# Kernel tuning notes

Measured on AMD Instinct MI355X. Metric: run time of the kernel, lower is better.

The kernel has to match this reference:

```python
import jax, jax.numpy as jnp
import numpy as np

CE_W, TRI_W, CEN_W, ALN_W, BAL_W = 1.0, 1.0, 0.0005, 0.5, 0.1
LS_EPS = 0.1      # label smoothing
MARGIN = 0.3      # triplet margin
F_ALPHA, F_GAMMA = 0.25, 2.0


def setup_inputs() -> dict:
    key = jax.random.key(0)
    ks = jax.random.split(key, 7)
    B, C, D = 1024, 8000, 2048
    return {
        "logits": jax.random.normal(ks[0], (B, C), jnp.float32),
        "features": jax.random.normal(ks[1], (B, D), jnp.float32),
        "feat_rgb": jax.random.normal(ks[2], (B, D), jnp.float32),
        "feat_ir": jax.random.normal(ks[3], (B, D), jnp.float32),
        "modality_weights": jax.random.uniform(ks[4], (B, 2), jnp.float32),
        "centers": jax.random.uniform(ks[5], (C, D), jnp.float32, -1.0, 1.0),
        "labels": jax.random.randint(ks[6], (B,), 0, 64),
    }


def reference(logits, features, feat_rgb, feat_ir, modality_weights, centers, labels):
    B, C = logits.shape
    logp = jax.nn.log_softmax(logits, axis=-1)                      # [B, C]
    logp_y = jnp.take_along_axis(logp, labels[:, None], axis=1)[:, 0]
    # CrossEntropy with label smoothing 0.1 (torch semantics)
    ce = jnp.mean(-(1.0 - LS_EPS) * logp_y - LS_EPS * jnp.mean(logp, axis=-1))
    # Focal loss (faithful to source: uses logpt, so term is <= 0)
    ce_ns = -logp_y
    pt = jnp.exp(-ce_ns)
    focal = jnp.mean(F_ALPHA * (1.0 - pt) ** F_GAMMA * (-ce_ns))
    # Batch-hard triplet (vectorized replacement for per-row python loop)
    sq = jnp.sum(features ** 2, axis=1)
    d2 = jnp.maximum(sq[:, None] + sq[None, :] - 2.0 * (features @ features.T), 0.0)
    dist = jnp.where(d2 > 0, jnp.sqrt(jnp.where(d2 > 0, d2, 1.0)), 0.0)  # safe sqrt
    eq = labels[:, None] == labels[None, :]
    eye = jnp.eye(B, dtype=bool)
    pos_mask = eq & ~eye
    neg_mask = ~eq
    hp = jnp.max(jnp.where(pos_mask, dist, -1.0), axis=1)   # hardest positive
    hn = jnp.min(jnp.where(neg_mask, dist, 1e9), axis=1)    # hardest negative
    valid = jnp.any(pos_mask, axis=1) & jnp.any(neg_mask, axis=1)
    tl = jax.nn.relu(hp - hn + MARGIN)
    triplet = jnp.sum(jnp.where(valid, tl, 0.0)) / jnp.maximum(jnp.sum(valid), 1)
    # Center loss (centers gathered and detached)
    cen = jnp.mean((features - jax.lax.stop_gradient(centers[labels])) ** 2)
    # Modality alignment (single rgb-ir pair): mean(1 - cos)
    f1 = feat_rgb / jnp.maximum(jnp.linalg.norm(feat_rgb, axis=1, keepdims=True), 1e-12)
    f2 = feat_ir / jnp.maximum(jnp.linalg.norm(feat_ir, axis=1, keepdims=True), 1e-12)
    align = jnp.mean(1.0 - jnp.sum(f1 * f2, axis=1))
    # Modality balance: max_entropy - entropy
    ent = jnp.mean(-jnp.sum(modality_weights * jnp.log(modality_weights + 1e-8), axis=1))
    balance = jnp.log(jnp.float32(modality_weights.shape[1])) - ent
    # Modality consistency: mse to detached mean over modalities
    mean_feat = jax.lax.stop_gradient(0.5 * (feat_rgb + feat_ir))
    cons = 0.5 * (jnp.mean((feat_rgb - mean_feat) ** 2) + jnp.mean((feat_ir - mean_feat) ** 2))
    total = (CE_W * (0.7 * ce + 0.3 * focal) + TRI_W * triplet + CEN_W * cen
             + ALN_W * align + BAL_W * balance + 0.1 * cons)
    return jnp.stack([total, ce, focal, triplet, cen, align, balance, cons])
```

## Files before the change

kernel.cpp:

```cpp
#include <hip/hip_runtime.h>
#include <math.h>

#define NB 1024
#define NC 8000
#define ND 2048

#define WS_SQ   0
#define WS_CE   1024
#define WS_FO   2048
#define WS_CEN  3072
#define WS_AL   4096
#define WS_CO   5120
#define WS_HPM  6144
#define WS_HNM  22528
#define WS_FB_BYTES 262144

#define NDIST 512

typedef __attribute__((ext_vector_type(8))) short bf16x8;
typedef __attribute__((ext_vector_type(4))) float f32x4;
#define GLOB __attribute__((address_space(1)))
#define LDSP __attribute__((address_space(3)))

__device__ inline unsigned short f2bf(float f) {
    unsigned u = __float_as_uint(f);
    u += 0x7FFFu + ((u >> 16) & 1u);
    return (unsigned short)(u >> 16);
}

__global__ __launch_bounds__(256) void k_feat(const float* __restrict__ F,
                                              const float* __restrict__ RGB,
                                              const float* __restrict__ IR,
                                              const float* __restrict__ CEN,
                                              const int* __restrict__ labels,
                                              float* __restrict__ ws,
                                              unsigned short* __restrict__ Fb) {
    const int tid = threadIdx.x;
    const int lane = tid & 63, wid = tid >> 6;
    const int row = blockIdx.x * 4 + wid;
    const float4* f4 = (const float4*)(F + (size_t)row * ND);
    const float4* c4 = (const float4*)(CEN + (size_t)labels[row] * ND);
    const float4* r4 = (const float4*)(RGB + (size_t)row * ND);
    const float4* g4 = (const float4*)(IR + (size_t)row * ND);
    ushort4* fb4 = (ushort4*)(Fb + (size_t)row * ND);

    float s_ff = 0, s_fc = 0, s_rr = 0, s_ii = 0, s_ri = 0, s_dd = 0;
#pragma unroll 4
    for (int t = 0; t < (ND / 4) / 64; ++t) {
        const int q = t * 64 + lane;
        float4 f = f4[q], c = c4[q], r = r4[q], g = g4[q];
        ushort4 h;
        h.x = f2bf(f.x); h.y = f2bf(f.y); h.z = f2bf(f.z); h.w = f2bf(f.w);
        fb4[q] = h;
        float fa[4] = {f.x, f.y, f.z, f.w};
        float ca[4] = {c.x, c.y, c.z, c.w};
        float ra[4] = {r.x, r.y, r.z, r.w};
        float ga[4] = {g.x, g.y, g.z, g.w};
#pragma unroll
        for (int k = 0; k < 4; ++k) {
            s_ff = fmaf(fa[k], fa[k], s_ff);
            float d = fa[k] - ca[k];
            s_fc = fmaf(d, d, s_fc);
            s_rr = fmaf(ra[k], ra[k], s_rr);
            s_ii = fmaf(ga[k], ga[k], s_ii);
            s_ri = fmaf(ra[k], ga[k], s_ri);
            float e = ra[k] - ga[k];
            s_dd = fmaf(e, e, s_dd);
        }
    }
#pragma unroll
    for (int off = 32; off > 0; off >>= 1) {
        s_ff += __shfl_down(s_ff, off);
        s_fc += __shfl_down(s_fc, off);
        s_rr += __shfl_down(s_rr, off);
        s_ii += __shfl_down(s_ii, off);
        s_ri += __shfl_down(s_ri, off);
        s_dd += __shfl_down(s_dd, off);
    }
    if (lane == 0) {
        ws[WS_SQ + row] = s_ff;
        ws[WS_CEN + row] = s_fc;
        float nr = fmaxf(sqrtf(s_rr), 1e-12f);
        float ni = fmaxf(sqrtf(s_ii), 1e-12f);
        ws[WS_AL + row] = 1.0f - s_ri / (nr * ni);
        ws[WS_CO + row] = s_dd;
    }
}

__global__ __launch_bounds__(256) void k_main(const unsigned short* __restrict__ Fb,
                                              const float* __restrict__ logits,
                                              const int* __restrict__ labels,
                                              float* __restrict__ ws) {
    __shared__ __align__(16) unsigned short As[2][32 * 64];
    __shared__ __align__(16) unsigned short Bs[2][64 * 64];
    __shared__ int lr[32], lc[64];
    __shared__ float sqr[32], sqc[64], hpl[32], hnl[32];
    __shared__ float rs[4], rsx[4];

    const int tid = threadIdx.x;
    const int lane = tid & 63, wid = tid >> 6;

    if (blockIdx.x < NDIST) {
        const int cb = blockIdx.x & 15;
        const int row0 = (blockIdx.x >> 4) << 5;
        const int col0 = cb << 6;
        const float* sq = ws + WS_SQ;

        if (tid < 32) {
            lr[tid] = labels[row0 + tid];
            sqr[tid] = sq[row0 + tid];
            hpl[tid] = -1.0f;
            hnl[tid] = 1e9f;
        } else if (tid >= 64 && tid < 128) {
            int t = tid - 64;
            lc[t] = labels[col0 + t];
            sqc[t] = sq[col0 + t];
        }

        const int r8 = lane >> 3;
        const int sl = lane & 7;
        const int soEl = ((sl ^ r8) * 8);

#define STAGE(IT, BUF) do {                                                              \
    const int k0_ = (IT) * 64;                                                           \
    __builtin_amdgcn_global_load_lds(                                                    \
        (const GLOB unsigned int*)(Fb + (size_t)(row0 + wid * 8 + r8) * ND + k0_ + soEl),\
        (LDSP unsigned int*)&As[BUF][(wid * 8) * 64], 16, 0, 0);                         \
    _Pragma("unroll")                                                                    \
    for (int t = 0; t < 2; ++t) {                                                        \
        const int rb_ = wid * 16 + t * 8;                                                \
        __builtin_amdgcn_global_load_lds(                                                \
            (const GLOB unsigned int*)(Fb + (size_t)(col0 + rb_ + r8) * ND + k0_ + soEl),\
            (LDSP unsigned int*)&Bs[BUF][rb_ * 64], 16, 0, 0);                           \
    }                                                                                    \
} while (0)

        const int wr = wid >> 1, wc = wid & 1;
        f32x4 acc[2] = {};

        STAGE(0, 0);
        int cur = 0;
        for (int it = 0; it < ND / 64; ++it) {
            __syncthreads();
            if (it + 1 < ND / 64) STAGE(it + 1, cur ^ 1);
            const char* Ab = (const char*)&As[cur][0];
            const char* Bb = (const char*)&Bs[cur][0];
#pragma unroll
            for (int kk = 0; kk < 2; ++kk) {
                const int kb = kk * 64 + (lane >> 4) * 16;
                const int xo = (lane & 7) << 4;
                const int rt = wr * 16 + (lane & 15);
                bf16x8 a = *(const bf16x8*)(Ab + rt * 128 + (kb ^ xo));
                bf16x8 b[2];
#pragma unroll
                for (int ni = 0; ni < 2; ++ni) {
                    const int ct = wc * 32 + ni * 16 + (lane & 15);
                    b[ni] = *(const bf16x8*)(Bb + ct * 128 + (kb ^ xo));
                }
#pragma unroll
                for (int ni = 0; ni < 2; ++ni)
                    acc[ni] = __builtin_amdgcn_mfma_f32_16x16x32_bf16(a, b[ni], acc[ni], 0, 0, 0);
            }
            cur ^= 1;
        }
#undef STAGE

#pragma unroll
        for (int reg = 0; reg < 4; ++reg) {
            const int rt = wr * 16 + (lane >> 4) * 4 + reg;
            const int lbr = lr[rt];
            const float sr = sqr[rt];
            float myhp = -1.0f, myhn = 1e9f;
#pragma unroll
            for (int ni = 0; ni < 2; ++ni) {
                const int ct = wc * 32 + ni * 16 + (lane & 15);
                float d2 = sr + sqc[ct] - 2.0f * acc[ni][reg];
                float dist = sqrtf(fmaxf(d2, 0.0f));
                if (row0 + rt != col0 + ct) {
                    if (lbr == lc[ct]) myhp = fmaxf(myhp, dist);
                    else               myhn = fminf(myhn, dist);
                }
            }
#pragma unroll
            for (int off = 1; off < 16; off <<= 1) {
                myhp = fmaxf(myhp, __shfl_xor(myhp, off, 16));
                myhn = fminf(myhn, __shfl_xor(myhn, off, 16));
            }
            if ((lane & 15) == 0) {
                atomicMax((int*)&hpl[rt], __float_as_int(myhp));
                atomicMin((int*)&hnl[rt], __float_as_int(myhn));
            }
        }
        __syncthreads();
        if (tid < 32) {
            ws[WS_HPM + (size_t)(row0 + tid) * 16 + cb] = hpl[tid];
            ws[WS_HNM + (size_t)(row0 + tid) * 16 + cb] = hnl[tid];
        }
    } else {
        const int row = blockIdx.x - NDIST;
        const float* x = logits + (size_t)row * NC;
        const float4* x4 = (const float4*)x;
        float xl = 0.0f;
        if (tid == 0) xl = x[labels[row]];

        float s = 0.0f, sx = 0.0f;
        for (int q = tid; q < NC / 4; q += 256) {
            float4 v = x4[q];
            float vv[4] = {v.x, v.y, v.z, v.w};
#pragma unroll
            for (int c = 0; c < 4; ++c) {
                sx += vv[c];
                s += __expf(vv[c]);
            }
        }
#pragma unroll
        for (int off = 32; off > 0; off >>= 1) {
            s  += __shfl_down(s, off);
            sx += __shfl_down(sx, off);
        }
        if (lane == 0) { rs[wid] = s; rsx[wid] = sx; }
        __syncthreads();
        if (tid == 0) {
            s = rs[0] + rs[1] + rs[2] + rs[3];
            sx = rsx[0] + rsx[1] + rsx[2] + rsx[3];
            const float lse = __logf(s);
            const float logp_y = xl - lse;
            const float mean_logp = sx * (1.0f / NC) - lse;
            const float pt = __expf(logp_y);
            ws[WS_CE + row] = -(1.0f - 0.1f) * logp_y - 0.1f * mean_logp;
            ws[WS_FO + row] = 0.25f * (1.0f - pt) * (1.0f - pt) * logp_y;
        }
    }
}

__global__ __launch_bounds__(256) void k_fin(const float* __restrict__ mw,
                                             float* __restrict__ ws,
                                             float* __restrict__ out) {
    const int tid = threadIdx.x;
    float sum_tl = 0.0f, ent = 0.0f, sce = 0.0f, sfo = 0.0f;
    float scen = 0.0f, sal = 0.0f, sco = 0.0f;
    int cnt = 0;
#pragma unroll
    for (int t = 0; t < 4; ++t) {
        const int i = tid + t * 256;
        const float4* hp4 = (const float4*)(ws + WS_HPM + (size_t)i * 16);
        const float4* hn4 = (const float4*)(ws + WS_HNM + (size_t)i * 16);
        float h1 = -1.0f, h2 = 1e9f;
#pragma unroll
        for (int c = 0; c < 4; ++c) {
            float4 p = hp4[c], n = hn4[c];
            h1 = fmaxf(h1, fmaxf(fmaxf(p.x, p.y), fmaxf(p.z, p.w)));
            h2 = fminf(h2, fminf(fminf(n.x, n.y), fminf(n.z, n.w)));
        }
        if (h1 >= 0.0f && h2 < 1e8f) { sum_tl += fmaxf(h1 - h2 + 0.3f, 0.0f); cnt++; }
        sce += ws[WS_CE + i];
        sfo += ws[WS_FO + i];
        scen += ws[WS_CEN + i];
        sal += ws[WS_AL + i];
        sco += ws[WS_CO + i];
        float w0 = mw[2 * i], w1 = mw[2 * i + 1];
        ent -= w0 * __logf(w0 + 1e-8f) + w1 * __logf(w1 + 1e-8f);
    }
#pragma unroll
    for (int off = 32; off > 0; off >>= 1) {
        sum_tl += __shfl_down(sum_tl, off);
        ent += __shfl_down(ent, off);
        sce += __shfl_down(sce, off);
        sfo += __shfl_down(sfo, off);
        scen += __shfl_down(scen, off);
        sal += __shfl_down(sal, off);
        sco += __shfl_down(sco, off);
        cnt += __shfl_down(cnt, off);
    }
    __shared__ float red[4][7];
    __shared__ int rc[4];
    const int lane = tid & 63, wid = tid >> 6;
    if (lane == 0) {
        red[wid][0] = sum_tl; red[wid][1] = ent; red[wid][2] = sce; red[wid][3] = sfo;
        red[wid][4] = scen; red[wid][5] = sal; red[wid][6] = sco;
        rc[wid] = cnt;
    }
    __syncthreads();
    if (tid == 0) {
#pragma unroll
        for (int w = 1; w < 4; ++w) {
            red[0][0] += red[w][0]; red[0][1] += red[w][1]; red[0][2] += red[w][2];
            red[0][3] += red[w][3]; red[0][4] += red[w][4]; red[0][5] += red[w][5];
            red[0][6] += red[w][6];
            rc[0] += rc[w];
        }
        const float ce = red[0][2] * (1.0f / NB);
        const float focal = red[0][3] * (1.0f / NB);
        const float triplet = red[0][0] / (float)(rc[0] > 0 ? rc[0] : 1);
        const float cen = red[0][4] * (1.0f / ((float)NB * ND));
        const float align = red[0][5] * (1.0f / NB);
        const float balance = logf(2.0f) - red[0][1] * (1.0f / NB);
        const float cons = 0.25f * red[0][6] * (1.0f / ((float)NB * ND));
        const float total = 1.0f * (0.7f * ce + 0.3f * focal) + 1.0f * triplet
                          + 0.0005f * cen + 0.5f * align + 0.1f * balance + 0.1f * cons;
        out[0] = total; out[1] = ce; out[2] = focal; out[3] = triplet;
        out[4] = cen; out[5] = align; out[6] = balance; out[7] = cons;
    }
}

extern "C" void kernel_launch(void* const* d_in, const int* in_sizes, int n_in,
                              void* d_out, int out_size, void* d_ws, size_t ws_size,
                              hipStream_t stream) {
    const float* logits   = (const float*)d_in[0];
    const float* features = (const float*)d_in[1];
    const float* feat_rgb = (const float*)d_in[2];
    const float* feat_ir  = (const float*)d_in[3];
    const float* mw       = (const float*)d_in[4];
    const float* centers  = (const float*)d_in[5];
    const int*   labels   = (const int*)d_in[6];
    float* ws  = (float*)d_ws;
    unsigned short* Fb = (unsigned short*)((char*)d_ws + WS_FB_BYTES);
    float* out = (float*)d_out;

    k_feat<<<dim3(NB / 4), dim3(256), 0, stream>>>(features, feat_rgb, feat_ir,
                                                   centers, labels, ws, Fb);
    k_main<<<dim3(NDIST + NB), dim3(256), 0, stream>>>(Fb, logits, labels, ws);
    k_fin<<<dim3(1), dim3(256), 0, stream>>>(mw, ws, out);
}
```

Measured before the change: 42.49 us.

## Load MFMA operands directly from global memory and remap distance blocks per XCD

Drops the double-buffered LDS staging of the bf16 Gram-matrix tiles. Each lane now reads its bf16x8 fragments straight from global memory, relying on L2/cache reuse instead of shared memory. Distance block indices are also remapped so blocks landing on the same XCD share row and column panels, to improve L2 locality. This removes the per-iteration barriers and LDS traffic, but each loaded fragment feeds only two MFMAs, so the loop may become bound on global load latency.

```diff
diff --git a/kernel.cpp b/kernel.cpp
--- a/kernel.cpp
+++ b/kernel.cpp
@@ -19,8 +19,6 @@
 
 typedef __attribute__((ext_vector_type(8))) short bf16x8;
 typedef __attribute__((ext_vector_type(4))) float f32x4;
-#define GLOB __attribute__((address_space(1)))
-#define LDSP __attribute__((address_space(3)))
 
 __device__ inline unsigned short f2bf(float f) {
     unsigned u = __float_as_uint(f);
@@ -91,8 +89,6 @@
                                               const float* __restrict__ logits,
                                               const int* __restrict__ labels,
                                               float* __restrict__ ws) {
-    __shared__ __align__(16) unsigned short As[2][32 * 64];
-    __shared__ __align__(16) unsigned short Bs[2][64 * 64];
     __shared__ int lr[32], lc[64];
     __shared__ float sqr[32], sqc[64], hpl[32], hnl[32];
     __shared__ float rs[4], rsx[4];
@@ -101,9 +97,11 @@
     const int lane = tid & 63, wid = tid >> 6;
 
     if (blockIdx.x < NDIST) {
-        const int cb = blockIdx.x & 15;
-        const int row0 = (blockIdx.x >> 4) << 5;
-        const int col0 = cb << 6;
+        const int d = blockIdx.x;
+        const int xcd = d & 7, loc = d >> 3;
+        const int rp = (xcd >> 1) * 8 + (loc & 7);
+        const int cb = (xcd & 1) * 8 + (loc >> 3);
+        const int row0 = rp << 5, col0 = cb << 6;
         const float* sq = ws + WS_SQ;
 
         if (tid < 32) {
@@ -117,53 +115,23 @@
             sqc[t] = sq[col0 + t];
         }
 
-        const int r8 = lane >> 3;
-        const int sl = lane & 7;
-        const int soEl = ((sl ^ r8) * 8);
-
-#define STAGE(IT, BUF) do {                                                              \
-    const int k0_ = (IT) * 64;                                                           \
-    __builtin_amdgcn_global_load_lds(                                                    \
-        (const GLOB unsigned int*)(Fb + (size_t)(row0 + wid * 8 + r8) * ND + k0_ + soEl),\
-        (LDSP unsigned int*)&As[BUF][(wid * 8) * 64], 16, 0, 0);                         \
-    _Pragma("unroll")                                                                    \
-    for (int t = 0; t < 2; ++t) {                                                        \
-        const int rb_ = wid * 16 + t * 8;                                                \
-        __builtin_amdgcn_global_load_lds(                                                \
-            (const GLOB unsigned int*)(Fb + (size_t)(col0 + rb_ + r8) * ND + k0_ + soEl),\
-            (LDSP unsigned int*)&Bs[BUF][rb_ * 64], 16, 0, 0);                           \
-    }                                                                                    \
-} while (0)
-
         const int wr = wid >> 1, wc = wid & 1;
+        const int lane15 = lane & 15, kq = lane >> 4;
+        const unsigned short* pa  = Fb + (size_t)(row0 + wr * 16 + lane15) * ND + kq * 8;
+        const unsigned short* pb0 = Fb + (size_t)(col0 + wc * 32 + lane15) * ND + kq * 8;
+        const unsigned short* pb1 = pb0 + 16 * ND;
+
         f32x4 acc[2] = {};
-
-        STAGE(0, 0);
-        int cur = 0;
-        for (int it = 0; it < ND / 64; ++it) {
-            __syncthreads();
-            if (it + 1 < ND / 64) STAGE(it + 1, cur ^ 1);
-            const char* Ab = (const char*)&As[cur][0];
-            const char* Bb = (const char*)&Bs[cur][0];
-#pragma unroll
-            for (int kk = 0; kk < 2; ++kk) {
-                const int kb = kk * 64 + (lane >> 4) * 16;
-                const int xo = (lane & 7) << 4;
-                const int rt = wr * 16 + (lane & 15);
-                bf16x8 a = *(const bf16x8*)(Ab + rt * 128 + (kb ^ xo));
-                bf16x8 b[2];
-#pragma unroll
-                for (int ni = 0; ni < 2; ++ni) {
-                    const int ct = wc * 32 + ni * 16 + (lane & 15);
-                    b[ni] = *(const bf16x8*)(Bb + ct * 128 + (kb ^ xo));
-                }
-#pragma unroll
-                for (int ni = 0; ni < 2; ++ni)
-                    acc[ni] = __builtin_amdgcn_mfma_f32_16x16x32_bf16(a, b[ni], acc[ni], 0, 0, 0);
-            }
-            cur ^= 1;
-        }
-#undef STAGE
+#pragma unroll 8
+        for (int it = 0; it < ND / 32; ++it) {
+            bf16x8 a  = *(const bf16x8*)(pa  + it * 32);
+            bf16x8 b0 = *(const bf16x8*)(pb0 + it * 32);
+            bf16x8 b1 = *(const bf16x8*)(pb1 + it * 32);
+            acc[0] = __builtin_amdgcn_mfma_f32_16x16x32_bf16(a, b0, acc[0], 0, 0, 0);
+            acc[1] = __builtin_amdgcn_mfma_f32_16x16x32_bf16(a, b1, acc[1], 0, 0, 0);
+        }
+
+        __syncthreads();
 
 #pragma unroll
         for (int reg = 0; reg < 4; ++reg) {
@@ -317,8 +285,8 @@
     unsigned short* Fb = (unsigned short*)((char*)d_ws + WS_FB_BYTES);
     float* out = (float*)d_out;
 
-    k_feat<<<dim3(NB / 4), dim3(256), 0, stream>>>(features, feat_rgb, feat_ir,
-                                                   centers, labels, ws, Fb);
+    k_feat<<<dim3(256), dim3(256), 0, stream>>>(features, feat_rgb, feat_ir,
+                                                centers, labels, ws, Fb);
     k_main<<<dim3(NDIST + NB), dim3(256), 0, stream>>>(Fb, logits, labels, ws);
     k_fin<<<dim3(1), dim3(256), 0, stream>>>(mw, ws, out);
 }
```

Result: slower. 64.05 us (+50.8%).

## Exploit Gram-matrix symmetry with 64x64 upper-triangular tiles and padded bf16 rows

Applied to the files above, without the earlier changes.

The distance GEMM now computes only the upper-triangular 64x64 tiles (136 blocks instead of 512 32x64 blocks). Each off-diagonal tile also reduces along columns to produce the transposed row's hardest positive and negative. The bf16 feature rows are padded to a stride of 2080 to avoid channel or bank conflicts. The pipeline uses explicit vmcnt waits and raw barriers. This halves the GEMM work but leaves fewer, heavier blocks and adds a second per-tile reduction pass.

```diff
diff --git a/kernel.cpp b/kernel.cpp
--- a/kernel.cpp
+++ b/kernel.cpp
@@ -4,6 +4,7 @@
 #define NB 1024
 #define NC 8000
 #define ND 2048
+#define FBS 2080
 
 #define WS_SQ   0
 #define WS_CE   1024
@@ -15,7 +16,8 @@
 #define WS_HNM  22528
 #define WS_FB_BYTES 262144
 
-#define NDIST 512
+#define NTILES 136
+#define NT     32
 
 typedef __attribute__((ext_vector_type(8))) short bf16x8;
 typedef __attribute__((ext_vector_type(4))) float f32x4;
@@ -42,7 +44,7 @@
     const float4* c4 = (const float4*)(CEN + (size_t)labels[row] * ND);
     const float4* r4 = (const float4*)(RGB + (size_t)row * ND);
     const float4* g4 = (const float4*)(IR + (size_t)row * ND);
-    ushort4* fb4 = (ushort4*)(Fb + (size_t)row * ND);
+    ushort4* fb4 = (ushort4*)(Fb + (size_t)row * FBS);
 
     float s_ff = 0, s_fc = 0, s_rr = 0, s_ii = 0, s_ri = 0, s_dd = 0;
 #pragma unroll 4
@@ -91,30 +93,34 @@
                                               const float* __restrict__ logits,
                                               const int* __restrict__ labels,
                                               float* __restrict__ ws) {
-    __shared__ __align__(16) unsigned short As[2][32 * 64];
+    __shared__ __align__(16) unsigned short As[2][64 * 64];
     __shared__ __align__(16) unsigned short Bs[2][64 * 64];
-    __shared__ int lr[32], lc[64];
-    __shared__ float sqr[32], sqc[64], hpl[32], hnl[32];
+    __shared__ int lr[64], lc[64];
+    __shared__ float sqr[64], sqc[64];
+    __shared__ float hplR[64], hnlR[64], hplC[64], hnlC[64];
     __shared__ float rs[4], rsx[4];
 
     const int tid = threadIdx.x;
     const int lane = tid & 63, wid = tid >> 6;
 
-    if (blockIdx.x < NDIST) {
-        const int cb = blockIdx.x & 15;
-        const int row0 = (blockIdx.x >> 4) << 5;
-        const int col0 = cb << 6;
+    if (blockIdx.x < NTILES) {
+        int rem = blockIdx.x, rp = 0;
+        while (rem >= 16 - rp) { rem -= 16 - rp; rp++; }
+        const int cp = rp + rem;
+        const int row0 = rp << 6, col0 = cp << 6;
         const float* sq = ws + WS_SQ;
 
-        if (tid < 32) {
+        if (tid < 64) {
             lr[tid] = labels[row0 + tid];
             sqr[tid] = sq[row0 + tid];
-            hpl[tid] = -1.0f;
-            hnl[tid] = 1e9f;
-        } else if (tid >= 64 && tid < 128) {
+            hplR[tid] = -1.0f;
+            hnlR[tid] = 1e9f;
+        } else if (tid < 128) {
             int t = tid - 64;
             lc[t] = labels[col0 + t];
             sqc[t] = sq[col0 + t];
+            hplC[t] = -1.0f;
+            hnlC[t] = 1e9f;
         }
 
         const int r8 = lane >> 3;
@@ -123,81 +129,133 @@
 
 #define STAGE(IT, BUF) do {                                                              \
     const int k0_ = (IT) * 64;                                                           \
-    __builtin_amdgcn_global_load_lds(                                                    \
-        (const GLOB unsigned int*)(Fb + (size_t)(row0 + wid * 8 + r8) * ND + k0_ + soEl),\
-        (LDSP unsigned int*)&As[BUF][(wid * 8) * 64], 16, 0, 0);                         \
     _Pragma("unroll")                                                                    \
     for (int t = 0; t < 2; ++t) {                                                        \
         const int rb_ = wid * 16 + t * 8;                                                \
         __builtin_amdgcn_global_load_lds(                                                \
-            (const GLOB unsigned int*)(Fb + (size_t)(col0 + rb_ + r8) * ND + k0_ + soEl),\
+            (const GLOB unsigned int*)(Fb + (size_t)(row0 + rb_ + r8) * FBS + k0_ + soEl),\
+            (LDSP unsigned int*)&As[BUF][rb_ * 64], 16, 0, 0);                           \
+        __builtin_amdgcn_global_load_lds(                                                \
+            (const GLOB unsigned int*)(Fb + (size_t)(col0 + rb_ + r8) * FBS + k0_ + soEl),\
             (LDSP unsigned int*)&Bs[BUF][rb_ * 64], 16, 0, 0);                           \
     }                                                                                    \
 } while (0)
 
         const int wr = wid >> 1, wc = wid & 1;
-        f32x4 acc[2] = {};
+        f32x4 acc[2][2] = {};
 
         STAGE(0, 0);
         int cur = 0;
-        for (int it = 0; it < ND / 64; ++it) {
-            __syncthreads();
-            if (it + 1 < ND / 64) STAGE(it + 1, cur ^ 1);
+#pragma unroll 1
+        for (int it = 0; it < NT; ++it) {
+            if (it + 1 < NT) {
+                STAGE(it + 1, cur ^ 1);
+                asm volatile("s_waitcnt vmcnt(4)" ::: "memory");
+            } else {
+                asm volatile("s_waitcnt vmcnt(0)" ::: "memory");
+            }
+            __builtin_amdgcn_sched_barrier(0);
+            __builtin_amdgcn_s_barrier();
+
             const char* Ab = (const char*)&As[cur][0];
             const char* Bb = (const char*)&Bs[cur][0];
 #pragma unroll
             for (int kk = 0; kk < 2; ++kk) {
                 const int kb = kk * 64 + (lane >> 4) * 16;
                 const int xo = (lane & 7) << 4;
-                const int rt = wr * 16 + (lane & 15);
-                bf16x8 a = *(const bf16x8*)(Ab + rt * 128 + (kb ^ xo));
-                bf16x8 b[2];
+                bf16x8 a[2], b[2];
+#pragma unroll
+                for (int mi = 0; mi < 2; ++mi) {
+                    const int rt = wr * 32 + mi * 16 + (lane & 15);
+                    a[mi] = *(const bf16x8*)(Ab + rt * 128 + (kb ^ xo));
+                }
 #pragma unroll
                 for (int ni = 0; ni < 2; ++ni) {
                     const int ct = wc * 32 + ni * 16 + (lane & 15);
                     b[ni] = *(const bf16x8*)(Bb + ct * 128 + (kb ^ xo));
                 }
 #pragma unroll
-                for (int ni = 0; ni < 2; ++ni)
-                    acc[ni] = __builtin_amdgcn_mfma_f32_16x16x32_bf16(a, b[ni], acc[ni], 0, 0, 0);
-            }
+                for (int mi = 0; mi < 2; ++mi)
+#pragma unroll
+                    for (int ni = 0; ni < 2; ++ni)
+                        acc[mi][ni] = __builtin_amdgcn_mfma_f32_16x16x32_bf16(a[mi], b[ni], acc[mi][ni], 0, 0, 0);
+            }
+
+            __builtin_amdgcn_sched_barrier(0);
+            __builtin_amdgcn_s_barrier();
             cur ^= 1;
         }
 #undef STAGE
 
 #pragma unroll
-        for (int reg = 0; reg < 4; ++reg) {
-            const int rt = wr * 16 + (lane >> 4) * 4 + reg;
-            const int lbr = lr[rt];
-            const float sr = sqr[rt];
-            float myhp = -1.0f, myhn = 1e9f;
+        for (int mi = 0; mi < 2; ++mi) {
+#pragma unroll
+            for (int reg = 0; reg < 4; ++reg) {
+                const int rt = wr * 32 + mi * 16 + (lane >> 4) * 4 + reg;
+                const int lbr = lr[rt];
+                const float sr = sqr[rt];
+                float myhp = -1.0f, myhn = 1e9f;
+#pragma unroll
+                for (int ni = 0; ni < 2; ++ni) {
+                    const int ct = wc * 32 + ni * 16 + (lane & 15);
+                    float d2 = sr + sqc[ct] - 2.0f * acc[mi][ni][reg];
+                    float dist = sqrtf(fmaxf(d2, 0.0f));
+                    if (row0 + rt != col0 + ct) {
+                        if (lbr == lc[ct]) myhp = fmaxf(myhp, dist);
+                        else               myhn = fminf(myhn, dist);
+                    }
+                }
+#pragma unroll
+                for (int off = 1; off < 16; off <<= 1) {
+                    myhp = fmaxf(myhp, __shfl_xor(myhp, off, 16));
+                    myhn = fminf(myhn, __shfl_xor(myhn, off, 16));
+                }
+                if ((lane & 15) == 0) {
+                    atomicMax((int*)&hplR[rt], __float_as_int(myhp));
+                    atomicMin((int*)&hnlR[rt], __float_as_int(myhn));
+                }
+            }
+        }
+
+        if (rp != cp) {
 #pragma unroll
             for (int ni = 0; ni < 2; ++ni) {
                 const int ct = wc * 32 + ni * 16 + (lane & 15);
-                float d2 = sr + sqc[ct] - 2.0f * acc[ni][reg];
-                float dist = sqrtf(fmaxf(d2, 0.0f));
-                if (row0 + rt != col0 + ct) {
-                    if (lbr == lc[ct]) myhp = fmaxf(myhp, dist);
-                    else               myhn = fminf(myhn, dist);
-                }
-            }
-#pragma unroll
-            for (int off = 1; off < 16; off <<= 1) {
-                myhp = fmaxf(myhp, __shfl_xor(myhp, off, 16));
-                myhn = fminf(myhn, __shfl_xor(myhn, off, 16));
-            }
-            if ((lane & 15) == 0) {
-                atomicMax((int*)&hpl[rt], __float_as_int(myhp));
-                atomicMin((int*)&hnl[rt], __float_as_int(myhn));
+                const int lbc = lc[ct];
+                const float sc = sqc[ct];
+                float myhp = -1.0f, myhn = 1e9f;
+#pragma unroll
+                for (int mi = 0; mi < 2; ++mi) {
+#pragma unroll
+                    for (int reg = 0; reg < 4; ++reg) {
+                        const int rt = wr * 32 + mi * 16 + (lane >> 4) * 4 + reg;
+                        float d2 = sqr[rt] + sc - 2.0f * acc[mi][ni][reg];
+                        float dist = sqrtf(fmaxf(d2, 0.0f));
+                        if (lr[rt] == lbc) myhp = fmaxf(myhp, dist);
+                        else               myhn = fminf(myhn, dist);
+                    }
+                }
+                myhp = fmaxf(myhp, __shfl_xor(myhp, 16));
+                myhn = fminf(myhn, __shfl_xor(myhn, 16));
+                myhp = fmaxf(myhp, __shfl_xor(myhp, 32));
+                myhn = fminf(myhn, __shfl_xor(myhn, 32));
+                if ((lane >> 4) == 0) {
+                    atomicMax((int*)&hplC[ct], __float_as_int(myhp));
+                    atomicMin((int*)&hnlC[ct], __float_as_int(myhn));
+                }
             }
         }
         __syncthreads();
-        if (tid < 32) {
-            ws[WS_HPM + (size_t)(row0 + tid) * 16 + cb] = hpl[tid];
-            ws[WS_HNM + (size_t)(row0 + tid) * 16 + cb] = hnl[tid];
+        if (tid < 64) {
+            ws[WS_HPM + (size_t)(row0 + tid) * 16 + cp] = hplR[tid];
+            ws[WS_HNM + (size_t)(row0 + tid) * 16 + cp] = hnlR[tid];
+        } else if (tid < 128 && rp != cp) {
+            int t = tid - 64;
+            ws[WS_HPM + (size_t)(col0 + t) * 16 + rp] = hplC[t];
+            ws[WS_HNM + (size_t)(col0 + t) * 16 + rp] = hnlC[t];
         }
     } else {
-        const int row = blockIdx.x - NDIST;
+        const int row = blockIdx.x - NTILES;
         const float* x = logits + (size_t)row * NC;
         const float4* x4 = (const float4*)x;
         float xl = 0.0f;
@@ -317,8 +375,8 @@
     unsigned short* Fb = (unsigned short*)((char*)d_ws + WS_FB_BYTES);
     float* out = (float*)d_out;
 
-    k_feat<<<dim3(NB / 4), dim3(256), 0, stream>>>(features, feat_rgb, feat_ir,
-                                                   centers, labels, ws, Fb);
-    k_main<<<dim3(NDIST + NB), dim3(256), 0, stream>>>(Fb, logits, labels, ws);
+    k_feat<<<dim3(256), dim3(256), 0, stream>>>(features, feat_rgb, feat_ir,
+                                                centers, labels, ws, Fb);
+    k_main<<<dim3(NTILES + NB), dim3(256), 0, stream>>>(Fb, logits, labels, ws);
     k_fin<<<dim3(1), dim3(256), 0, stream>>>(mw, ws, out);
 }
```

After: 43.08 us. Within noise of the previous version (+1.4%).
